# Kernel tuning notes

Hardware: AMD Instinct MI355X
Metric: run time of the kernel (lower is better)

The kernel has to match this reference:

```python
import jax, jax.numpy as jnp
import numpy as np

B = 256   # number of segments
P = 2000  # points per segment (hard-coded by fc_1 = Linear(2000*32, 1024))
C = 32    # point feature channels
EPS_BN = 1e-5


def _bn_relu(h, g, b):
    # BatchNorm1d in training mode: batch statistics over axis 0, biased variance.
    m = jnp.mean(h, axis=0)
    v = jnp.var(h, axis=0)
    return jax.nn.relu((h - m) * jax.lax.rsqrt(v + EPS_BN) * g + b)


def setup_inputs() -> dict:
    key = jax.random.key(0)
    ks = jax.random.split(key, 16)
    s = 0.02
    inp = {
        "x": jax.random.normal(ks[0], (B * P, C), jnp.float32),
        "length": jnp.full((B,), P, dtype=jnp.int32),
        # attention MLP (1x1 conv1d chain 32->16->8->1), torch layout [out,in]
        "w1": jax.random.normal(ks[1], (16, 32), jnp.float32) * s,
        "b1": jnp.zeros((16,), jnp.float32),
        "g1": jnp.ones((16,), jnp.float32),
        "be1": jnp.zeros((16,), jnp.float32),
        "w2": jax.random.normal(ks[2], (8, 16), jnp.float32) * s,
        "b2": jnp.zeros((8,), jnp.float32),
        "g2": jnp.ones((8,), jnp.float32),
        "be2": jnp.zeros((8,), jnp.float32),
        "w3": jax.random.normal(ks[3], (1, 8), jnp.float32) * s,
        "b3": jnp.zeros((1,), jnp.float32),
        "g3": jnp.ones((1,), jnp.float32),
        "be3": jnp.zeros((1,), jnp.float32),
        # FC head
        "fw1": jax.random.normal(ks[4], (1024, P * C), jnp.float32) * s,
        "fb1": jnp.zeros((1024,), jnp.float32),
        "fg1": jnp.ones((1024,), jnp.float32),
        "fbe1": jnp.zeros((1024,), jnp.float32),
        "fw2": jax.random.normal(ks[5], (256, 1024), jnp.float32) * s,
        "fb2": jnp.zeros((256,), jnp.float32),
        "fg2": jnp.ones((256,), jnp.float32),
        "fbe2": jnp.zeros((256,), jnp.float32),
    }
    return inp


def reference(x, length, w1, b1, g1, be1, w2, b2, g2, be2, w3, b3, g3, be3,
              fw1, fb1, fg1, fbe1, fw2, fb2, fg2, fbe2):
    # Pointwise attention score MLP over all points (BN stats over the full
    # point dimension, matching conv1d+BatchNorm1d with batch size 1).
    h = _bn_relu(x @ w1.T + b1, g1, be1)          # [N,16]
    h = _bn_relu(h @ w2.T + b2, g2, be2)          # [N,8]
    score = _bn_relu(h @ w3.T + b3, g3, be3)      # [N,1]

    # Per-segment softmax over the point dim, then weighted features + flatten.
    # All segments have exactly P=2000 points (required by fc_1's input dim),
    # so the ragged slicing collapses to a dense [B,P,*] reshape.
    att = jax.nn.softmax(score.reshape(B, P, 1), axis=1)   # [B,P,1]
    pooled = (x.reshape(B, P, C) * att).reshape(B, P * C)  # [B,64000]

    r = _bn_relu(pooled @ fw1.T + fb1, fg1, fbe1)  # [B,1024]
    r = _bn_relu(r @ fw2.T + fb2, fg2, fbe2)       # [B,256]

    # F.normalize(p=2, dim=1, eps=1e-12)
    norm = jnp.maximum(jnp.linalg.norm(r, axis=1, keepdims=True), 1e-12)
    return r / norm
```

## Files before the change

kernel.cpp:

```cpp
#include <hip/hip_runtime.h>
#include <hip/hip_bf16.h>

#define NPTS   512000
#define PSEG   2000
#define INV_N  (1.0f/512000.0f)
#define EPS_BN 1e-5f

#define S1_OFF 0
#define S2_OFF 1024
#define S3_OFF 1536
#define S4_OFF 1600
#define S5_OFF 9792

using u32 = unsigned int;
using u16 = unsigned short;
using f32x4  = __attribute__((ext_vector_type(4))) float;
using bf16x8 = __attribute__((ext_vector_type(8))) short;

static __device__ __forceinline__ u16 f2bf(float f) {
    u32 u = __builtin_bit_cast(u32, f);
    u += 0x7fffu + ((u >> 16) & 1u);
    return (u16)(u >> 16);
}

static __device__ __forceinline__ void gload_lds16(const void* g, void* l) {
    __builtin_amdgcn_global_load_lds(
        (const __attribute__((address_space(1))) unsigned int*)g,
        (__attribute__((address_space(3))) unsigned int*)l, 16, 0, 0);
}

__global__ __launch_bounds__(256) void k_zero(float4* __restrict__ p) {
    p[blockIdx.x * 256 + threadIdx.x] = float4{0.0f, 0.0f, 0.0f, 0.0f};
}

__global__ __launch_bounds__(256) void k_mlp1(const float* __restrict__ x,
                                              const float* __restrict__ w1,
                                              float* __restrict__ a1,
                                              float* __restrict__ stats) {
    __shared__ float w[512];
    __shared__ float part[4][32];
    const int t = threadIdx.x;
    w[t] = w1[t]; w[t + 256] = w1[t + 256];
    __syncthreads();

    const int idx = blockIdx.x * 256 + t;
    const float4* xr = (const float4*)(x + (size_t)idx * 32);
    float4 xv[8];
#pragma unroll
    for (int i = 0; i < 8; i++) xv[i] = xr[i];

    float h[16];
#pragma unroll
    for (int c = 0; c < 16; c++) {
        float s = 0.0f;
        const float4* wr = (const float4*)(w + c * 32);
#pragma unroll
        for (int i = 0; i < 8; i++) {
            float4 wv = wr[i];
            s += xv[i].x * wv.x + xv[i].y * wv.y + xv[i].z * wv.z + xv[i].w * wv.w;
        }
        h[c] = s;
    }

    float4* ar = (float4*)(a1 + (size_t)idx * 16);
#pragma unroll
    for (int i = 0; i < 4; i++) {
        float4 o; o.x = h[i*4+0]; o.y = h[i*4+1]; o.z = h[i*4+2]; o.w = h[i*4+3];
        ar[i] = o;
    }

    const int lane = t & 63, wave = t >> 6;
#pragma unroll
    for (int c = 0; c < 16; c++) {
        float s = h[c], q = h[c] * h[c];
#pragma unroll
        for (int off = 32; off > 0; off >>= 1) {
            s += __shfl_down(s, off);
            q += __shfl_down(q, off);
        }
        if (lane == 0) { part[wave][c] = s; part[wave][16 + c] = q; }
    }
    __syncthreads();
    if (t < 32) {
        float tot = part[0][t] + part[1][t] + part[2][t] + part[3][t];
        atomicAdd(&stats[S1_OFF + (blockIdx.x & 31) * 32 + t], tot);
    }
}

__global__ __launch_bounds__(256) void k_mlp2(const float* __restrict__ a1,
                                              const float* __restrict__ w2,
                                              const float* __restrict__ g1,
                                              const float* __restrict__ be1,
                                              float* __restrict__ a2,
                                              float* __restrict__ stats) {
    __shared__ float w[128];
    __shared__ float sc[16], sh[16];
    __shared__ float part[4][16];
    const int t = threadIdx.x;
    if (t < 128) w[t] = w2[t];
    if (t < 16) {
        float s = 0.0f, q = 0.0f;
#pragma unroll 8
        for (int c = 0; c < 32; c++) {
            s += stats[S1_OFF + c * 32 + t];
            q += stats[S1_OFF + c * 32 + 16 + t];
        }
        float m = s * INV_N;
        float v = q * INV_N - m * m;
        float sl = g1[t] * rsqrtf(v + EPS_BN);
        sc[t] = sl; sh[t] = be1[t] - m * sl;
    }
    __syncthreads();

    const int idx = blockIdx.x * 256 + t;
    const float4* ar = (const float4*)(a1 + (size_t)idx * 16);
    float h[16];
#pragma unroll
    for (int i = 0; i < 4; i++) {
        float4 v4 = ar[i];
        h[i*4+0] = v4.x; h[i*4+1] = v4.y; h[i*4+2] = v4.z; h[i*4+3] = v4.w;
    }
#pragma unroll
    for (int c = 0; c < 16; c++) h[c] = fmaxf(fmaf(h[c], sc[c], sh[c]), 0.0f);

    float o[8];
#pragma unroll
    for (int c = 0; c < 8; c++) {
        float s = 0.0f;
#pragma unroll
        for (int k = 0; k < 16; k++) s += h[k] * w[c * 16 + k];
        o[c] = s;
    }
    float4* orp = (float4*)(a2 + (size_t)idx * 8);
    float4 o0; o0.x=o[0]; o0.y=o[1]; o0.z=o[2]; o0.w=o[3];
    float4 o1; o1.x=o[4]; o1.y=o[5]; o1.z=o[6]; o1.w=o[7];
    orp[0] = o0; orp[1] = o1;

    const int lane = t & 63, wave = t >> 6;
#pragma unroll
    for (int c = 0; c < 8; c++) {
        float s = o[c], q = o[c] * o[c];
#pragma unroll
        for (int off = 32; off > 0; off >>= 1) {
            s += __shfl_down(s, off);
            q += __shfl_down(q, off);
        }
        if (lane == 0) { part[wave][c] = s; part[wave][8 + c] = q; }
    }
    __syncthreads();
    if (t < 16) {
        float tot = part[0][t] + part[1][t] + part[2][t] + part[3][t];
        atomicAdd(&stats[S2_OFF + (blockIdx.x & 31) * 16 + t], tot);
    }
}

__global__ __launch_bounds__(256) void k_mlp3(const float* __restrict__ a2,
                                              const float* __restrict__ w3,
                                              const float* __restrict__ g2,
                                              const float* __restrict__ be2,
                                              float* __restrict__ a3,
                                              float* __restrict__ stats) {
    __shared__ float w[8], sc[8], sh[8];
    __shared__ float part[4][2];
    const int t = threadIdx.x;
    if (t < 8) {
        w[t] = w3[t];
        float s = 0.0f, q = 0.0f;
#pragma unroll 8
        for (int c = 0; c < 32; c++) {
            s += stats[S2_OFF + c * 16 + t];
            q += stats[S2_OFF + c * 16 + 8 + t];
        }
        float m = s * INV_N;
        float v = q * INV_N - m * m;
        float sl = g2[t] * rsqrtf(v + EPS_BN);
        sc[t] = sl; sh[t] = be2[t] - m * sl;
    }
    __syncthreads();

    const int idx = blockIdx.x * 256 + t;
    const float4* ar = (const float4*)(a2 + (size_t)idx * 8);
    float4 v0 = ar[0], v1 = ar[1];
    float h[8] = {v0.x, v0.y, v0.z, v0.w, v1.x, v1.y, v1.z, v1.w};
    float s = 0.0f;
#pragma unroll
    for (int c = 0; c < 8; c++) s += fmaxf(fmaf(h[c], sc[c], sh[c]), 0.0f) * w[c];
    a3[idx] = s;

    const int lane = t & 63, wave = t >> 6;
    float q = s * s;
    float ss = s;
#pragma unroll
    for (int off = 32; off > 0; off >>= 1) {
        ss += __shfl_down(ss, off);
        q  += __shfl_down(q, off);
    }
    if (lane == 0) { part[wave][0] = ss; part[wave][1] = q; }
    __syncthreads();
    if (t < 2) {
        float tot = part[0][t] + part[1][t] + part[2][t] + part[3][t];
        atomicAdd(&stats[S3_OFF + (blockIdx.x & 31) * 2 + t], tot);
    }
}

__global__ __launch_bounds__(256) void k_pool(const float* __restrict__ a3,
                                              const float* __restrict__ x,
                                              const float* __restrict__ g3,
                                              const float* __restrict__ be3,
                                              const float* __restrict__ stats,
                                              u16* __restrict__ pooled) {
    const int b = blockIdx.x, t = threadIdx.x;
    float sm = 0.0f, sq = 0.0f;
#pragma unroll 8
    for (int c = 0; c < 32; c++) {
        sm += stats[S3_OFF + c * 2];
        sq += stats[S3_OFF + c * 2 + 1];
    }
    const float m  = sm * INV_N;
    const float v  = sq * INV_N - m * m;
    const float sc = g3[0] * rsqrtf(v + EPS_BN);
    const float sh = be3[0] - m * sc;

    float sv[8];
    float mx = -1e30f;
#pragma unroll
    for (int i = 0; i < 8; i++) {
        int p = t + i * 256;
        if (p < PSEG) {
            float val = fmaxf(fmaf(a3[(size_t)b * PSEG + p], sc, sh), 0.0f);
            sv[i] = val; mx = fmaxf(mx, val);
        } else sv[i] = -1e30f;
    }
    const int lane = t & 63, wave = t >> 6;
    __shared__ float redm[4], reds[4];
#pragma unroll
    for (int off = 32; off > 0; off >>= 1) mx = fmaxf(mx, __shfl_xor(mx, off));
    if (lane == 0) redm[wave] = mx;
    __syncthreads();
    mx = fmaxf(fmaxf(redm[0], redm[1]), fmaxf(redm[2], redm[3]));

    float es = 0.0f;
#pragma unroll
    for (int i = 0; i < 8; i++) {
        int p = t + i * 256;
        if (p < PSEG) { float e = __expf(sv[i] - mx); sv[i] = e; es += e; }
    }
#pragma unroll
    for (int off = 32; off > 0; off >>= 1) es += __shfl_xor(es, off);
    if (lane == 0) reds[wave] = es;
    __syncthreads();
    const float inv = 1.0f / (reds[0] + reds[1] + reds[2] + reds[3]);

    const int swz = (b & 7) << 3;
#pragma unroll
    for (int i = 0; i < 8; i++) {
        int p = t + i * 256;
        if (p >= PSEG) continue;
        const float att = sv[i] * inv;
        const float4* xr = (const float4*)(x + ((size_t)b * PSEG + p) * 32);
        u16* dst = pooled + (size_t)b * 64000 + (size_t)(p >> 1) * 64;
        const int half = (p & 1) << 5;
#pragma unroll
        for (int u = 0; u < 4; u++) {
            float4 f0 = xr[u * 2], f1 = xr[u * 2 + 1];
            u32 q0 = (u32)f2bf(f0.x * att) | ((u32)f2bf(f0.y * att) << 16);
            u32 q1 = (u32)f2bf(f0.z * att) | ((u32)f2bf(f0.w * att) << 16);
            u32 q2 = (u32)f2bf(f1.x * att) | ((u32)f2bf(f1.y * att) << 16);
            u32 q3 = (u32)f2bf(f1.z * att) | ((u32)f2bf(f1.w * att) << 16);
            uint4 q; q.x = q0; q.y = q1; q.z = q2; q.w = q3;
            *(uint4*)(dst + ((half | (u << 3)) ^ swz)) = q;
        }
    }
}

__global__ __launch_bounds__(256) void k_gemm4(const u16* __restrict__ pooled,
                                               const float* __restrict__ fw1,
                                               float* __restrict__ a4p) {
    __shared__ alignas(16) char smem[81920];

    const int t = threadIdx.x;
    const int jblk = blockIdx.x;
    const int kblk = blockIdx.y;
    const int wave = t >> 6, lane = t & 63;
    const int kbase = kblk * 1600;

    const u16* gA = pooled + (size_t)(wave * 8 + (lane >> 3)) * 64000 + (lane & 7) * 8 + kbase;
    const int jj = t >> 4;
    const int ks = (t & 15) * 4;
    const float* gB = fw1 + (size_t)(jblk * 64 + jj) * 64000 + ks + kbase;

    f32x4 acc[4][4] = {};
    float4 b0, b1, b2, b3;

#define ISSUE_B(STEP) {                                                       \
        const float* bs = gB + (STEP) * 64;                                   \
        b0 = *(const float4*)(bs);                                            \
        b1 = *(const float4*)(bs + (size_t)16 * 64000);                       \
        b2 = *(const float4*)(bs + (size_t)32 * 64000);                       \
        b3 = *(const float4*)(bs + (size_t)48 * 64000); }
#define ISSUE_A(STEP, BUF) {                                                  \
        _Pragma("unroll")                                                     \
        for (int i = 0; i < 8; i++)                                           \
            gload_lds16(gA + (STEP) * 64 + (size_t)i * 32 * 64000,            \
                        smem + (BUF) * 32768 + wave * 1024 + i * 4096); }
#define WRITE_B(BUF) {                                                        \
        char* Bw = smem + 65536 + (BUF) * 8192;                               \
        _Pragma("unroll")                                                     \
        for (int i = 0; i < 4; i++) {                                         \
            const int j = i * 16 + jj;                                        \
            float4 v = (i == 0) ? b0 : (i == 1) ? b1 : (i == 2) ? b2 : b3;    \
            ushort4 bv;                                                       \
            bv.x = f2bf(v.x); bv.y = f2bf(v.y);                               \
            bv.z = f2bf(v.z); bv.w = f2bf(v.w);                               \
            *(ushort4*)(Bw + ((j * 128 + ks * 2) ^ ((j & 7) << 4))) = bv; } }

    ISSUE_B(0);
    __builtin_amdgcn_sched_barrier(0);
    ISSUE_A(0, 0);
    __builtin_amdgcn_sched_barrier(0);
    asm volatile("s_waitcnt vmcnt(8)" ::: "memory");
    __builtin_amdgcn_sched_barrier(0);
    WRITE_B(0);
    ISSUE_B(1);
    __builtin_amdgcn_sched_barrier(0);
    ISSUE_A(1, 1);
    __builtin_amdgcn_sched_barrier(0);
    asm volatile("s_waitcnt vmcnt(12) lgkmcnt(0)" ::: "memory");
    __builtin_amdgcn_sched_barrier(0);
    __builtin_amdgcn_s_barrier();

    int cur = 0;
#pragma unroll 1
    for (int step = 0; step < 25; ++step) {
        const char* As = smem + cur * 32768;
        const char* Bs = smem + 65536 + cur * 8192;
        __builtin_amdgcn_s_setprio(1);
#pragma unroll
        for (int kk = 0; kk < 2; ++kk) {
            const int krow = kk * 32 + (lane >> 4) * 8;
            bf16x8 aF[4], bF[4];
#pragma unroll
            for (int mm = 0; mm < 4; mm++) {
                const int row = wave * 64 + mm * 16 + (lane & 15);
                aF[mm] = *(const bf16x8*)(As + ((row * 128 + krow * 2) ^ ((row & 7) << 4)));
            }
#pragma unroll
            for (int nn = 0; nn < 4; nn++) {
                const int col = nn * 16 + (lane & 15);
                bF[nn] = *(const bf16x8*)(Bs + ((col * 128 + krow * 2) ^ ((col & 7) << 4)));
            }
#pragma unroll
            for (int mm = 0; mm < 4; mm++)
#pragma unroll
                for (int nn = 0; nn < 4; nn++)
                    acc[mm][nn] = __builtin_amdgcn_mfma_f32_16x16x32_bf16(
                        aF[mm], bF[nn], acc[mm][nn], 0, 0, 0);
        }
        __builtin_amdgcn_s_setprio(0);
        __builtin_amdgcn_sched_barrier(0);
        __builtin_amdgcn_s_barrier();
        __builtin_amdgcn_sched_barrier(0);
        if (step + 1 < 25) {
            asm volatile("s_waitcnt vmcnt(8)" ::: "memory");
            __builtin_amdgcn_sched_barrier(0);
            WRITE_B(cur ^ 1);
            __builtin_amdgcn_sched_barrier(0);
            if (step + 2 < 25) {
                ISSUE_B(step + 2);
                __builtin_amdgcn_sched_barrier(0);
                ISSUE_A(step + 2, cur);
                __builtin_amdgcn_sched_barrier(0);
                asm volatile("s_waitcnt vmcnt(12) lgkmcnt(0)" ::: "memory");
            } else {
                asm volatile("s_waitcnt vmcnt(0) lgkmcnt(0)" ::: "memory");
            }
            __builtin_amdgcn_sched_barrier(0);
            __builtin_amdgcn_s_barrier();
            __builtin_amdgcn_sched_barrier(0);
        }
        cur ^= 1;
    }
#undef ISSUE_B
#undef ISSUE_A
#undef WRITE_B

    float* dst = a4p + (size_t)kblk * 262144;
#pragma unroll
    for (int mm = 0; mm < 4; mm++)
#pragma unroll
        for (int nn = 0; nn < 4; nn++)
#pragma unroll
            for (int r = 0; r < 4; r++) {
                const int row = wave * 64 + mm * 16 + (lane >> 4) * 4 + r;
                const int col = jblk * 64 + nn * 16 + (lane & 15);
                dst[(size_t)row * 1024 + col] = acc[mm][nn][r];
            }
}

__global__ __launch_bounds__(256) void k_red4(const float* __restrict__ a4p,
                                              float* __restrict__ a4,
                                              float* __restrict__ stats) {
    const int i = blockIdx.x, t = threadIdx.x;
    float4 s = {0.0f, 0.0f, 0.0f, 0.0f};
#pragma unroll 8
    for (int kb = 0; kb < 40; kb++) {
        float4 v = *(const float4*)(a4p + (size_t)kb * 262144 + (size_t)i * 1024 + t * 4);
        s.x += v.x; s.y += v.y; s.z += v.z; s.w += v.w;
    }
    *(float4*)(a4 + (size_t)i * 1024 + t * 4) = s;
    const int j = t * 4;
    float* s4 = stats + S4_OFF + (i & 3) * 2048;
    atomicAdd(&s4[j + 0], s.x);
    atomicAdd(&s4[j + 1], s.y);
    atomicAdd(&s4[j + 2], s.z);
    atomicAdd(&s4[j + 3], s.w);
    atomicAdd(&s4[1024 + j + 0], s.x * s.x);
    atomicAdd(&s4[1024 + j + 1], s.y * s.y);
    atomicAdd(&s4[1024 + j + 2], s.z * s.z);
    atomicAdd(&s4[1024 + j + 3], s.w * s.w);
}

__global__ __launch_bounds__(256) void k_fc2(const float* __restrict__ a4,
                                             const float* __restrict__ fg1,
                                             const float* __restrict__ fbe1,
                                             const float* __restrict__ fw2,
                                             float* __restrict__ stats,
                                             float* __restrict__ a5) {
    __shared__ alignas(16) float h[1024];
    const int i = blockIdx.x, t = threadIdx.x;
#pragma unroll
    for (int u = 0; u < 4; u++) {
        const int k = u * 256 + t;
        float s = 0.0f, q = 0.0f;
#pragma unroll
        for (int c = 0; c < 4; c++) {
            s += stats[S4_OFF + c * 2048 + k];
            q += stats[S4_OFF + c * 2048 + 1024 + k];
        }
        float m  = s * (1.0f / 256.0f);
        float v  = q * (1.0f / 256.0f) - m * m;
        float sc = fg1[k] * rsqrtf(v + EPS_BN);
        float sh = fbe1[k] - m * sc;
        h[k] = fmaxf(fmaf(a4[(size_t)i * 1024 + k], sc, sh), 0.0f);
    }
    __syncthreads();
    const float4* wr = (const float4*)(fw2 + (size_t)t * 1024);
    const float4* hr = (const float4*)h;
    float s = 0.0f;
#pragma unroll 4
    for (int u = 0; u < 256; u++) {
        float4 w = wr[u], hv = hr[u];
        s += w.x * hv.x + w.y * hv.y + w.z * hv.z + w.w * hv.w;
    }
    a5[(size_t)i * 256 + t] = s;
    float* s5 = stats + S5_OFF + (i & 15) * 512;
    atomicAdd(&s5[t], s);
    atomicAdd(&s5[256 + t], s * s);
}

__global__ __launch_bounds__(256) void k_norm(const float* __restrict__ a5,
                                              const float* __restrict__ fg2,
                                              const float* __restrict__ fbe2,
                                              const float* __restrict__ stats,
                                              float* __restrict__ out) {
    const int i = blockIdx.x, t = threadIdx.x;
    float s = 0.0f, q2 = 0.0f;
#pragma unroll
    for (int c = 0; c < 16; c++) {
        s  += stats[S5_OFF + c * 512 + t];
        q2 += stats[S5_OFF + c * 512 + 256 + t];
    }
    float m  = s * (1.0f / 256.0f);
    float v  = q2 * (1.0f / 256.0f) - m * m;
    float sc = fg2[t] * rsqrtf(v + EPS_BN);
    float sh = fbe2[t] - m * sc;
    float r = fmaxf(fmaf(a5[(size_t)i * 256 + t], sc, sh), 0.0f);

    float q = r * r;
    const int lane = t & 63, wave = t >> 6;
#pragma unroll
    for (int off = 32; off > 0; off >>= 1) q += __shfl_xor(q, off);
    __shared__ float red[4];
    if (lane == 0) red[wave] = q;
    __syncthreads();
    float tot = red[0] + red[1] + red[2] + red[3];
    float nrm = fmaxf(sqrtf(tot), 1e-12f);
    out[(size_t)i * 256 + t] = r / nrm;
}

extern "C" void kernel_launch(void* const* d_in, const int* in_sizes, int n_in,
                              void* d_out, int out_size, void* d_ws, size_t ws_size,
                              hipStream_t stream) {
    const float* x   = (const float*)d_in[0];
    const float* w1  = (const float*)d_in[2];
    const float* g1  = (const float*)d_in[4];
    const float* be1 = (const float*)d_in[5];
    const float* w2  = (const float*)d_in[6];
    const float* g2  = (const float*)d_in[8];
    const float* be2 = (const float*)d_in[9];
    const float* w3  = (const float*)d_in[10];
    const float* g3  = (const float*)d_in[12];
    const float* be3 = (const float*)d_in[13];
    const float* fw1 = (const float*)d_in[14];
    const float* fg1 = (const float*)d_in[16];
    const float* fbe1= (const float*)d_in[17];
    const float* fw2 = (const float*)d_in[18];
    const float* fg2 = (const float*)d_in[20];
    const float* fbe2= (const float*)d_in[21];
    float* out = (float*)d_out;

    char* ws = (char*)d_ws;
    float* stats = (float*)ws;
    float* a4 = (float*)(ws + 73728);
    float* a5 = (float*)(ws + 73728 + 1048576);
    float* a4p = (float*)(ws + 73728 + 1048576 + 262144);
    char*  big = ws + 73728 + 1048576 + 262144 + 41943040;
    float* a1 = (float*)big;
    u16*   pooled = (u16*)big;
    float* a2 = (float*)(big + 32768000);
    float* a3 = (float*)(big + 32768000 + 16384000);

    k_zero<<<18, 256, 0, stream>>>((float4*)ws);
    k_mlp1<<<2000, 256, 0, stream>>>(x, w1, a1, stats);
    k_mlp2<<<2000, 256, 0, stream>>>(a1, w2, g1, be1, a2, stats);
    k_mlp3<<<2000, 256, 0, stream>>>(a2, w3, g2, be2, a3, stats);
    k_pool<<<256, 256, 0, stream>>>(a3, x, g3, be3, stats, pooled);
    k_gemm4<<<dim3(16, 40), 256, 0, stream>>>(pooled, fw1, a4p);
    k_red4<<<256, 256, 0, stream>>>(a4p, a4, stats);
    k_fc2<<<256, 256, 0, stream>>>(a4, fg1, fbe1, fw2, stats, a5);
    k_norm<<<256, 256, 0, stream>>>(a5, fg2, fbe2, stats, out);
}
```

Before: 267.0 us.

## Widen FC1 GEMM tile to 256x128 with 8 waves and single-buffered A

The fw1 GEMM block now covers 128 output columns with 512 threads arranged as a 4x2 wave grid, halving the grid width so each pooled A tile is loaded half as often overall. A is now single-buffered in LDS and B double-buffered, with a simpler prefetch schedule: B register loads are issued before compute, and A loads are issued after the barrier. That ordering leaves A loads unoverlapped with compute and waits with vmcnt(0), trading memory-latency hiding for lower A traffic and reduced LDS use.

```diff
diff --git a/kernel.cpp b/kernel.cpp
--- a/kernel.cpp
+++ b/kernel.cpp
@@ -273,67 +273,66 @@
     }
 }
 
-__global__ __launch_bounds__(256) void k_gemm4(const u16* __restrict__ pooled,
+__global__ __launch_bounds__(512) void k_gemm4(const u16* __restrict__ pooled,
                                                const float* __restrict__ fw1,
                                                float* __restrict__ a4p) {
-    __shared__ alignas(16) char smem[81920];
+    __shared__ alignas(16) char smem[65536];
 
     const int t = threadIdx.x;
     const int jblk = blockIdx.x;
     const int kblk = blockIdx.y;
     const int wave = t >> 6, lane = t & 63;
+    const int wm = wave >> 1, wn = wave & 1;
     const int kbase = kblk * 1600;
 
-    const u16* gA = pooled + (size_t)(wave * 8 + (lane >> 3)) * 64000 + (lane & 7) * 8 + kbase;
-    const int jj = t >> 4;
-    const int ks = (t & 15) * 4;
-    const float* gB = fw1 + (size_t)(jblk * 64 + jj) * 64000 + ks + kbase;
+    const u16* gA = pooled + (size_t)(wave * 8 + (lane >> 3)) * 64000
+                    + (lane & 7) * 8 + kbase;
+    const int jj = t >> 2, ksf = (t & 3) * 16;
+    const float* gB = fw1 + (size_t)(jblk * 128 + jj) * 64000 + ksf + kbase;
 
     f32x4 acc[4][4] = {};
     float4 b0, b1, b2, b3;
 
+#define ISSUE_A(STEP) {                                                       \
+        _Pragma("unroll")                                                     \
+        for (int i = 0; i < 4; i++)                                           \
+            gload_lds16(gA + (STEP) * 64 + (size_t)i * 64 * 64000,            \
+                        smem + i * 8192 + wave * 1024); }
 #define ISSUE_B(STEP) {                                                       \
         const float* bs = gB + (STEP) * 64;                                   \
         b0 = *(const float4*)(bs);                                            \
-        b1 = *(const float4*)(bs + (size_t)16 * 64000);                       \
-        b2 = *(const float4*)(bs + (size_t)32 * 64000);                       \
-        b3 = *(const float4*)(bs + (size_t)48 * 64000); }
-#define ISSUE_A(STEP, BUF) {                                                  \
+        b1 = *(const float4*)(bs + 4);                                        \
+        b2 = *(const float4*)(bs + 8);                                        \
+        b3 = *(const float4*)(bs + 12); }
+#define WRITE_B(BUF) {                                                        \
+        char* Bw = smem + 32768 + (BUF) * 16384;                              \
+        float f[16] = {b0.x,b0.y,b0.z,b0.w, b1.x,b1.y,b1.z,b1.w,              \
+                       b2.x,b2.y,b2.z,b2.w, b3.x,b3.y,b3.z,b3.w};             \
         _Pragma("unroll")                                                     \
-        for (int i = 0; i < 8; i++)                                           \
-            gload_lds16(gA + (STEP) * 64 + (size_t)i * 32 * 64000,            \
-                        smem + (BUF) * 32768 + wave * 1024 + i * 4096); }
-#define WRITE_B(BUF) {                                                        \
-        char* Bw = smem + 65536 + (BUF) * 8192;                               \
-        _Pragma("unroll")                                                     \
-        for (int i = 0; i < 4; i++) {                                         \
-            const int j = i * 16 + jj;                                        \
-            float4 v = (i == 0) ? b0 : (i == 1) ? b1 : (i == 2) ? b2 : b3;    \
-            ushort4 bv;                                                       \
-            bv.x = f2bf(v.x); bv.y = f2bf(v.y);                               \
-            bv.z = f2bf(v.z); bv.w = f2bf(v.w);                               \
-            *(ushort4*)(Bw + ((j * 128 + ks * 2) ^ ((j & 7) << 4))) = bv; } }
-
+        for (int u = 0; u < 2; u++) {                                         \
+            u32 q0 = (u32)f2bf(f[u*8+0]) | ((u32)f2bf(f[u*8+1]) << 16);       \
+            u32 q1 = (u32)f2bf(f[u*8+2]) | ((u32)f2bf(f[u*8+3]) << 16);       \
+            u32 q2 = (u32)f2bf(f[u*8+4]) | ((u32)f2bf(f[u*8+5]) << 16);       \
+            u32 q3 = (u32)f2bf(f[u*8+6]) | ((u32)f2bf(f[u*8+7]) << 16);      \
+            uint4 q; q.x = q0; q.y = q1; q.z = q2; q.w = q3;                  \
+            *(uint4*)(Bw + ((jj * 128 + ((t & 3) * 2 + u) * 16)               \
+                            ^ ((jj & 7) << 4))) = q; } }
+
+    ISSUE_A(0);
     ISSUE_B(0);
+    WRITE_B(0);
+    asm volatile("s_waitcnt vmcnt(0) lgkmcnt(0)" ::: "memory");
+    __builtin_amdgcn_s_barrier();
     __builtin_amdgcn_sched_barrier(0);
-    ISSUE_A(0, 0);
-    __builtin_amdgcn_sched_barrier(0);
-    asm volatile("s_waitcnt vmcnt(8)" ::: "memory");
-    __builtin_amdgcn_sched_barrier(0);
-    WRITE_B(0);
-    ISSUE_B(1);
-    __builtin_amdgcn_sched_barrier(0);
-    ISSUE_A(1, 1);
-    __builtin_amdgcn_sched_barrier(0);
-    asm volatile("s_waitcnt vmcnt(12) lgkmcnt(0)" ::: "memory");
-    __builtin_amdgcn_sched_barrier(0);
-    __builtin_amdgcn_s_barrier();
 
     int cur = 0;
 #pragma unroll 1
     for (int step = 0; step < 25; ++step) {
-        const char* As = smem + cur * 32768;
-        const char* Bs = smem + 65536 + cur * 8192;
+        const bool pf = (step + 1 < 25);
+        if (pf) ISSUE_B(step + 1);
+        __builtin_amdgcn_sched_barrier(0);
+        const char* As = smem;
+        const char* Bs = smem + 32768 + cur * 16384;
         __builtin_amdgcn_s_setprio(1);
 #pragma unroll
         for (int kk = 0; kk < 2; ++kk) {
@@ -341,12 +340,12 @@
             bf16x8 aF[4], bF[4];
 #pragma unroll
             for (int mm = 0; mm < 4; mm++) {
-                const int row = wave * 64 + mm * 16 + (lane & 15);
+                const int row = wm * 64 + mm * 16 + (lane & 15);
                 aF[mm] = *(const bf16x8*)(As + ((row * 128 + krow * 2) ^ ((row & 7) << 4)));
             }
 #pragma unroll
             for (int nn = 0; nn < 4; nn++) {
-                const int col = nn * 16 + (lane & 15);
+                const int col = wn * 64 + nn * 16 + (lane & 15);
                 bF[nn] = *(const bf16x8*)(Bs + ((col * 128 + krow * 2) ^ ((col & 7) << 4)));
             }
 #pragma unroll
@@ -360,28 +359,19 @@
         __builtin_amdgcn_sched_barrier(0);
         __builtin_amdgcn_s_barrier();
         __builtin_amdgcn_sched_barrier(0);
-        if (step + 1 < 25) {
-            asm volatile("s_waitcnt vmcnt(8)" ::: "memory");
+        if (pf) {
+            ISSUE_A(step + 1);
             __builtin_amdgcn_sched_barrier(0);
             WRITE_B(cur ^ 1);
             __builtin_amdgcn_sched_barrier(0);
-            if (step + 2 < 25) {
-                ISSUE_B(step + 2);
-                __builtin_amdgcn_sched_barrier(0);
-                ISSUE_A(step + 2, cur);
-                __builtin_amdgcn_sched_barrier(0);
-                asm volatile("s_waitcnt vmcnt(12) lgkmcnt(0)" ::: "memory");
-            } else {
-                asm volatile("s_waitcnt vmcnt(0) lgkmcnt(0)" ::: "memory");
-            }
-            __builtin_amdgcn_sched_barrier(0);
+            asm volatile("s_waitcnt vmcnt(0) lgkmcnt(0)" ::: "memory");
             __builtin_amdgcn_s_barrier();
             __builtin_amdgcn_sched_barrier(0);
         }
         cur ^= 1;
     }
+#undef ISSUE_A
 #undef ISSUE_B
-#undef ISSUE_A
 #undef WRITE_B
 
     float* dst = a4p + (size_t)kblk * 262144;
@@ -391,8 +381,8 @@
         for (int nn = 0; nn < 4; nn++)
 #pragma unroll
             for (int r = 0; r < 4; r++) {
-                const int row = wave * 64 + mm * 16 + (lane >> 4) * 4 + r;
-                const int col = jblk * 64 + nn * 16 + (lane & 15);
+                const int row = wm * 64 + mm * 16 + (lane >> 4) * 4 + r;
+                const int col = jblk * 128 + wn * 64 + nn * 16 + (lane & 15);
                 dst[(size_t)row * 1024 + col] = acc[mm][nn][r];
             }
 }
@@ -525,7 +515,7 @@
     k_mlp2<<<2000, 256, 0, stream>>>(a1, w2, g1, be1, a2, stats);
     k_mlp3<<<2000, 256, 0, stream>>>(a2, w3, g2, be2, a3, stats);
     k_pool<<<256, 256, 0, stream>>>(a3, x, g3, be3, stats, pooled);
-    k_gemm4<<<dim3(16, 40), 256, 0, stream>>>(pooled, fw1, a4p);
+    k_gemm4<<<dim3(8, 40), 512, 0, stream>>>(pooled, fw1, a4p);
     k_red4<<<256, 256, 0, stream>>>(a4p, a4, stats);
     k_fc2<<<256, 256, 0, stream>>>(a4, fg1, fbe1, fw2, stats, a5);
     k_norm<<<256, 256, 0, stream>>>(a5, fg2, fbe2, stats, out);
```

Measured after the change: 305.1 us. 14.3% more time.
